# Optimization experiments

Hardware: AMD Instinct MI355X
Metric: run time of the kernel (lower is better)

The kernel has to match this reference:

```python
import jax, jax.numpy as jnp
import numpy as np

D_MODEL = 1024
NUM_HEADS = 16
HEAD_DIM = D_MODEL // NUM_HEADS
SCALE = HEAD_DIM ** -0.5
LN_EPS = 1e-5
Q_EPS = 1e-5


def bit_quant(W):
    # BitNet b1.58 ternary weight quantization with straight-through estimator.
    gamma = jnp.mean(jnp.abs(W))
    Wq = jnp.clip(jnp.round(W / (gamma + Q_EPS)), -1.0, 1.0) * gamma
    return W + jax.lax.stop_gradient(Wq - W)


def layer_norm(x, gamma, beta):
    mu = jnp.mean(x, axis=-1, keepdims=True)
    var = jnp.mean(jnp.square(x - mu), axis=-1, keepdims=True)
    return (x - mu) * jax.lax.rsqrt(var + LN_EPS) * gamma + beta


def setup_inputs() -> dict:
    key = jax.random.key(0)
    ks = jax.random.split(key, 8)
    B, T, T_ctx, C = 4, 1024, 2048, D_MODEL
    w_std = C ** -0.5
    return {
        "x": jax.random.normal(ks[0], (B, T, C), jnp.float32),
        "context": jax.random.normal(ks[1], (B, T_ctx, C), jnp.float32),
        "Wq": jax.random.normal(ks[2], (C, C), jnp.float32) * w_std,
        "bq": jnp.zeros((C,), jnp.float32),
        "Wk": jax.random.normal(ks[3], (C, C), jnp.float32) * w_std,
        "bk": jnp.zeros((C,), jnp.float32),
        "Wv": jax.random.normal(ks[4], (C, C), jnp.float32) * w_std,
        "bv": jnp.zeros((C,), jnp.float32),
        "Wo": jax.random.normal(ks[5], (C, C), jnp.float32) * w_std,
        "bo": jnp.zeros((C,), jnp.float32),
        "ln_gamma": jnp.ones((C,), jnp.float32),
        "ln_beta": jnp.zeros((C,), jnp.float32),
    }


def reference(x, context, Wq, bq, Wk, bk, Wv, bv, Wo, bo, ln_gamma, ln_beta):
    B, T, C = x.shape
    T_ctx = context.shape[1]
    residual = x
    xn = layer_norm(x, ln_gamma, ln_beta)
    # BitNet-quantized projections (torch Linear: y = x @ W.T + b)
    q = xn @ bit_quant(Wq).T + bq                      # [B,T,C]
    k = context @ bit_quant(Wk).T + bk                 # [B,T_ctx,C]
    v = context @ bit_quant(Wv).T + bv                 # [B,T_ctx,C]
    q = q.reshape(B, T, NUM_HEADS, HEAD_DIM)
    k = k.reshape(B, T_ctx, NUM_HEADS, HEAD_DIM)
    v = v.reshape(B, T_ctx, NUM_HEADS, HEAD_DIM)
    scores = jnp.einsum("bqhd,bkhd->bhqk", q, k) * SCALE   # [B,H,T,T_ctx]
    probs = jax.nn.softmax(scores, axis=-1)
    out = jnp.einsum("bhqk,bkhd->bqhd", probs, v).reshape(B, T, C)
    return residual + (out @ bit_quant(Wo).T + bo)
```

## Files before the change

kernel.cpp:

```cpp
#include <hip/hip_runtime.h>
#include <hip/hip_bf16.h>

typedef __attribute__((ext_vector_type(8))) short s8x;
typedef __attribute__((ext_vector_type(4))) float f4x;
typedef unsigned short u16;
typedef unsigned int u32;

#define T_ 1024
#define TC_ 2048
#define SCLOG2E 0.1803368801111243f

#define WAIT_VM(n) asm volatile("s_waitcnt vmcnt(" #n ")" ::: "memory")

__device__ __forceinline__ u16 f2bf(float f) {
    u32 u = __float_as_uint(f);
    return (u16)((u + 0x7fffu + ((u >> 16) & 1u)) >> 16);
}

#if defined(__has_builtin)
#if __has_builtin(__builtin_amdgcn_cvt_pk_bf16_f32)
#define HAVE_PK 1
#endif
#if __has_builtin(__builtin_amdgcn_permlane16_swap) && __has_builtin(__builtin_amdgcn_permlane32_swap)
#define HAVE_PLSWAP 1
#endif
#endif

__device__ __forceinline__ u32 pack2bf(float a, float b) {
#ifdef HAVE_PK
    typedef __attribute__((ext_vector_type(2))) __bf16 bf2t;
    bf2t r = __builtin_amdgcn_cvt_pk_bf16_f32(a, b);
    u32 u;
    __builtin_memcpy(&u, &r, 4);
    return u;
#else
    return (u32)f2bf(a) | ((u32)f2bf(b) << 16);
#endif
}

__device__ __forceinline__ void pswap32(u32& a, u32& b) {
#ifdef HAVE_PLSWAP
    typedef __attribute__((ext_vector_type(2))) unsigned int u2x;
    u2x r = __builtin_amdgcn_permlane32_swap(a, b, false, false);
    a = r.x; b = r.y;
#else
    asm("v_permlane32_swap_b32 %0, %1" : "+v"(a), "+v"(b));
#endif
}
__device__ __forceinline__ void pswap16(u32& a, u32& b) {
#ifdef HAVE_PLSWAP
    typedef __attribute__((ext_vector_type(2))) unsigned int u2x;
    u2x r = __builtin_amdgcn_permlane16_swap(a, b, false, false);
    a = r.x; b = r.y;
#else
    asm("v_permlane16_swap_b32 %0, %1" : "+v"(a), "+v"(b));
#endif
}

__device__ __forceinline__ void gload16(const void* g, void* l) {
    __builtin_amdgcn_global_load_lds((const __attribute__((address_space(1))) u32*)g,
                                     (__attribute__((address_space(3))) u32*)l, 16, 0, 0);
}

__global__ __launch_bounds__(256) void absmean_k(const float* __restrict__ W0, const float* __restrict__ W1,
                                                 const float* __restrict__ W2, const float* __restrict__ W3,
                                                 float* __restrict__ gsum) {
    int wi = blockIdx.y;
    const float* W = (wi == 0) ? W0 : (wi == 1) ? W1 : (wi == 2) ? W2 : W3;
    const int n4 = (1024 * 1024) / 4;
    float s = 0.f;
    int stride = gridDim.x * blockDim.x;
    for (int i = blockIdx.x * blockDim.x + threadIdx.x; i < n4; i += stride) {
        float4 v = ((const float4*)W)[i];
        s += fabsf(v.x) + fabsf(v.y) + fabsf(v.z) + fabsf(v.w);
    }
#pragma unroll
    for (int off = 32; off; off >>= 1) s += __shfl_down(s, off, 64);
    __shared__ float ps[4];
    if ((threadIdx.x & 63) == 0) ps[threadIdx.x >> 6] = s;
    __syncthreads();
    if (threadIdx.x == 0) atomicAdd(gsum + wi, ps[0] + ps[1] + ps[2] + ps[3]);
}

__global__ __launch_bounds__(256) void prep_k(
        const float* __restrict__ x, const float* __restrict__ lng, const float* __restrict__ lnb,
        u16* __restrict__ xn,
        const float* __restrict__ ctx, u16* __restrict__ ctxb,
        const float* __restrict__ W0, const float* __restrict__ W1,
        const float* __restrict__ W2, const float* __restrict__ W3,
        u16* __restrict__ D0, u16* __restrict__ D1, u16* __restrict__ D2, u16* __restrict__ D3,
        const float* __restrict__ gsum) {
    __shared__ float ps[8];
    int bx = blockIdx.x, t = threadIdx.x;
    if (bx < 4096) {
        int row = bx;
        float4 xv = ((const float4*)(x + (long)row * 1024))[t];
        float s = xv.x + xv.y + xv.z + xv.w;
        float s2 = xv.x * xv.x + xv.y * xv.y + xv.z * xv.z + xv.w * xv.w;
#pragma unroll
        for (int off = 32; off; off >>= 1) { s += __shfl_down(s, off, 64); s2 += __shfl_down(s2, off, 64); }
        if ((t & 63) == 0) { ps[t >> 6] = s; ps[4 + (t >> 6)] = s2; }
        __syncthreads();
        float S = ps[0] + ps[1] + ps[2] + ps[3];
        float S2 = ps[4] + ps[5] + ps[6] + ps[7];
        float mu = S * (1.f / 1024.f);
        float var = S2 * (1.f / 1024.f) - mu * mu;
        float rstd = rsqrtf(var + 1e-5f);
        float4 gv = ((const float4*)lng)[t];
        float4 bv = ((const float4*)lnb)[t];
        uint2 o;
        o.x = pack2bf((xv.x - mu) * rstd * gv.x + bv.x, (xv.y - mu) * rstd * gv.y + bv.y);
        o.y = pack2bf((xv.z - mu) * rstd * gv.z + bv.z, (xv.w - mu) * rstd * gv.w + bv.w);
        ((uint2*)(xn + (long)row * 1024))[t] = o;
    } else if (bx < 12288) {
        int i = (bx - 4096) * 256 + t;
        float4 v = ((const float4*)ctx)[i];
        uint2 o = {pack2bf(v.x, v.y), pack2bf(v.z, v.w)};
        ((uint2*)ctxb)[i] = o;
    } else {
        int wi = (bx - 12288) >> 10;
        const float* W = (wi == 0) ? W0 : (wi == 1) ? W1 : (wi == 2) ? W2 : W3;
        u16* D = (wi == 0) ? D0 : (wi == 1) ? D1 : (wi == 2) ? D2 : D3;
        float inv = 1.0f / (gsum[wi] * (1.0f / 1048576.0f) + 1e-5f);
        int i = ((bx - 12288) & 1023) * 256 + t;
        float4 wv = ((const float4*)W)[i];
        uint2 o;
        o.x = pack2bf(fminf(1.f, fmaxf(-1.f, rintf(wv.x * inv))),
                      fminf(1.f, fmaxf(-1.f, rintf(wv.y * inv))));
        o.y = pack2bf(fminf(1.f, fmaxf(-1.f, rintf(wv.z * inv))),
                      fminf(1.f, fmaxf(-1.f, rintf(wv.w * inv))));
        ((uint2*)D)[i] = o;
    }
}

__global__ __launch_bounds__(256) void gemm_fused(
        const u16* __restrict__ xn, const u16* __restrict__ ctxb,
        const u16* __restrict__ wtq, const u16* __restrict__ wtk, const u16* __restrict__ wtv,
        const float* __restrict__ bq, const float* __restrict__ bk, const float* __restrict__ bv,
        const float* __restrict__ gsum,
        u16* __restrict__ qb, u16* __restrict__ kb, u16* __restrict__ vtb) {
    __shared__ __align__(16) char smem[65536];
    int tid = threadIdx.x;
    int w = tid >> 6, l = tid & 63, lq = l & 15, lh = l >> 4;
    int wm = (w >> 1) * 64, wn = (w & 1) * 64;
    int bx = blockIdx.x;
    int xcd = bx & 7;
    int prob, m0, n0, gidx;
    const u16 *A, *Wt;
    const float* bias;
    float sc;
    if (bx < 256) {
        int local = bx >> 3;
        prob = 0; A = xn; Wt = wtq; bias = bq; sc = SCLOG2E; gidx = 0;
        m0 = (xcd * 4 + (local & 3)) * 128;
        n0 = (local >> 2) * 128;
    } else {
        int b = bx - 256;
        int local3 = b >> 3;
        int kv = local3 & 1;
        int idx = local3 >> 1;
        prob = 1 + kv; A = ctxb;
        Wt = kv ? wtv : wtk; bias = kv ? bv : bk; sc = 1.0f; gidx = 1 + kv;
        m0 = (xcd * 8 + (idx & 7)) * 128;
        n0 = (idx >> 3) * 128;
    }
    int sp = tid >> 3, ss = tid & 7;
    int st = ss ^ (sp & 7);
    int r0 = sp * 2 + (st >> 2), c0 = st & 3;
    const u16* Ag0 = A + (long)(m0 + r0) * 1024 + c0 * 8;
    const u16* Ag1 = Ag0 + 64 * 1024;
    const u16* Bg0 = Wt + (long)(n0 + r0) * 1024 + c0 * 8;
    const u16* Bg1 = Bg0 + 64 * 1024;
    int aoff[4], boff[4];
#pragma unroll
    for (int i = 0; i < 4; i++) {
        int ar = wm + i * 16 + lq, ap = ar >> 1;
        aoff[i] = ap * 128 + (((((ar & 1) << 2) | lh) ^ (ap & 7)) * 16);
        int br = wn + i * 16 + lq, bp = br >> 1;
        boff[i] = bp * 128 + (((((br & 1) << 2) | lh) ^ (bp & 7)) * 16);
    }
    f4x acc[4][4] = {};
#define STAGE_G(kt, buf)                                                   \
    {                                                                      \
        char* Ad = smem + (buf) * 32768;                                   \
        gload16(Ag0 + (kt) * 64, Ad + tid * 16);                           \
        gload16(Ag1 + (kt) * 64, Ad + 4096 + tid * 16);                    \
        gload16(Ag0 + (kt) * 64 + 32, Ad + 8192 + tid * 16);               \
        gload16(Ag1 + (kt) * 64 + 32, Ad + 12288 + tid * 16);              \
        gload16(Bg0 + (kt) * 64, Ad + 16384 + tid * 16);                   \
        gload16(Bg1 + (kt) * 64, Ad + 20480 + tid * 16);                   \
        gload16(Bg0 + (kt) * 64 + 32, Ad + 24576 + tid * 16);              \
        gload16(Bg1 + (kt) * 64 + 32, Ad + 28672 + tid * 16);              \
    }
    STAGE_G(0, 0);
    STAGE_G(1, 1);
#pragma unroll
    for (int kt = 0; kt < 16; kt++) {
        if (kt < 15) { WAIT_VM(8); } else { WAIT_VM(0); }
        __builtin_amdgcn_s_barrier();
        const char* Ac = smem + (kt & 1) * 32768;
        const char* Bc = Ac + 16384;
        s8x af[2][4], bfr[2][4];
#pragma unroll
        for (int h = 0; h < 2; h++)
#pragma unroll
            for (int i = 0; i < 4; i++) {
                af[h][i] = *(const s8x*)(Ac + h * 8192 + aoff[i]);
                bfr[h][i] = *(const s8x*)(Bc + h * 8192 + boff[i]);
            }
#pragma unroll
        for (int h = 0; h < 2; h++)
#pragma unroll
            for (int i = 0; i < 4; i++)
#pragma unroll
                for (int j = 0; j < 4; j++)
                    acc[i][j] = __builtin_amdgcn_mfma_f32_16x16x32_bf16(af[h][i], bfr[h][j], acc[i][j], 0, 0, 0);
        __builtin_amdgcn_s_barrier();
        if (kt + 2 < 16) STAGE_G(kt + 2, kt & 1);
    }
    float gamma = gsum[gidx] * (1.0f / 1048576.0f) * sc;
    if (prob < 2) {
        u16* outq = (prob == 0) ? qb : kb;
        int tshift = (prob == 0) ? 10 : 11;
        int tmask = (1 << tshift) - 1;
#pragma unroll
        for (int i = 0; i < 4; i++) {
            int gr = m0 + wm + i * 16 + lh * 4;
#pragma unroll
            for (int j = 0; j < 4; j++) {
                int gc = n0 + wn + j * 16 + lq;
                float bb = bias[gc] * sc;
                int h = gc >> 6, d = gc & 63;
#pragma unroll
                for (int r = 0; r < 4; r++) {
                    int row = gr + r;
                    int bidx = row >> tshift, tt = row & tmask;
                    outq[((((long)(bidx * 16 + h)) << tshift) + tt) * 64 + d] = f2bf(acc[i][j][r] * gamma + bb);
                }
            }
        }
    } else {
        __syncthreads();
        char* Ct = smem;
#pragma unroll
        for (int i = 0; i < 4; i++) {
            int tt = wm + i * 16 + lh * 4;
#pragma unroll
            for (int j = 0; j < 4; j++) {
                int c = wn + j * 16 + lq;
                float bb = bias[n0 + c];
                uint2 pk;
                pk.x = pack2bf(acc[i][j][0] * gamma + bb, acc[i][j][1] * gamma + bb);
                pk.y = pack2bf(acc[i][j][2] * gamma + bb, acc[i][j][3] * gamma + bb);
                int slot = (tt >> 3) ^ (c & 15);
                *(uint2*)(Ct + c * 256 + slot * 16 + (tt & 7) * 2) = pk;
            }
        }
        __syncthreads();
        int bb2 = m0 >> 11, t0 = m0 & 2047;
#pragma unroll
        for (int it = 0; it < 8; it++) {
            int e = it * 256 + tid;
            int c = e >> 4, ch = e & 15;
            int slot = ch ^ (c & 15);
            s8x v = *(const s8x*)(Ct + c * 256 + slot * 16);
            int gcg = n0 + c;
            int h = gcg >> 6, d = gcg & 63;
            *(s8x*)(vtb + ((long)((bb2 * 16 + h) * 64 + d)) * TC_ + t0 + ch * 8) = v;
        }
    }
}

__global__ __launch_bounds__(256) void gemm_o(const u16* __restrict__ A, const u16* __restrict__ Wt,
                                              const float* __restrict__ bias, const float* __restrict__ gsum,
                                              const float* __restrict__ residual, float* __restrict__ outr) {
    __shared__ __align__(16) char smem[49152];
    int tid = threadIdx.x;
    int w = tid >> 6, l = tid & 63, lq = l & 15, lh = l >> 4;
    int wm = (w >> 1) * 64, wn = (w & 1) * 32;
    int bx = blockIdx.x;
    int xcd = bx & 7, local = bx >> 3;
    int m0 = (xcd * 4 + (local & 3)) * 128;
    int n0 = (local >> 2) * 64;
    int sp = tid >> 3, ss = tid & 7;
    int st = ss ^ (sp & 7);
    int r0 = sp * 2 + (st >> 2), c0 = st & 3;
    const u16* Ag0 = A + (long)(m0 + r0) * 1024 + c0 * 8;
    const u16* Ag1 = Ag0 + 64 * 1024;
    const u16* Bg0 = Wt + (long)(n0 + r0) * 1024 + c0 * 8;
    int aoff[4], boff[2];
#pragma unroll
    for (int i = 0; i < 4; i++) {
        int ar = wm + i * 16 + lq, ap = ar >> 1;
        aoff[i] = ap * 128 + (((((ar & 1) << 2) | lh) ^ (ap & 7)) * 16);
    }
#pragma unroll
    for (int j = 0; j < 2; j++) {
        int br = wn + j * 16 + lq, bp = br >> 1;
        boff[j] = bp * 128 + (((((br & 1) << 2) | lh) ^ (bp & 7)) * 16);
    }
    f4x acc[4][2] = {};
#define STAGE_O(kt, buf)                                                   \
    {                                                                      \
        char* Ad = smem + (buf) * 24576;                                   \
        gload16(Ag0 + (kt) * 64, Ad + tid * 16);                           \
        gload16(Ag1 + (kt) * 64, Ad + 4096 + tid * 16);                    \
        gload16(Ag0 + (kt) * 64 + 32, Ad + 8192 + tid * 16);               \
        gload16(Ag1 + (kt) * 64 + 32, Ad + 12288 + tid * 16);              \
        gload16(Bg0 + (kt) * 64, Ad + 16384 + tid * 16);                   \
        gload16(Bg0 + (kt) * 64 + 32, Ad + 20480 + tid * 16);              \
    }
    STAGE_O(0, 0);
    STAGE_O(1, 1);
#pragma unroll
    for (int kt = 0; kt < 16; kt++) {
        if (kt < 15) { WAIT_VM(6); } else { WAIT_VM(0); }
        __builtin_amdgcn_s_barrier();
        const char* Ac = smem + (kt & 1) * 24576;
        const char* Bc = Ac + 16384;
        s8x af[2][4], bfr[2][2];
#pragma unroll
        for (int h = 0; h < 2; h++) {
#pragma unroll
            for (int i = 0; i < 4; i++) af[h][i] = *(const s8x*)(Ac + h * 8192 + aoff[i]);
#pragma unroll
            for (int j = 0; j < 2; j++) bfr[h][j] = *(const s8x*)(Bc + h * 4096 + boff[j]);
        }
#pragma unroll
        for (int h = 0; h < 2; h++)
#pragma unroll
            for (int i = 0; i < 4; i++)
#pragma unroll
                for (int j = 0; j < 2; j++)
                    acc[i][j] = __builtin_amdgcn_mfma_f32_16x16x32_bf16(af[h][i], bfr[h][j], acc[i][j], 0, 0, 0);
        __builtin_amdgcn_s_barrier();
        if (kt + 2 < 16) STAGE_O(kt + 2, kt & 1);
    }
    float gamma = gsum[3] * (1.0f / 1048576.0f);
#pragma unroll
    for (int i = 0; i < 4; i++) {
        int gr = m0 + wm + i * 16 + lh * 4;
#pragma unroll
        for (int j = 0; j < 2; j++) {
            int gc = n0 + wn + j * 16 + lq;
            float bb = bias[gc];
#pragma unroll
            for (int r = 0; r < 4; r++) {
                long idx = (long)(gr + r) * 1024 + gc;
                outr[idx] = residual[idx] + acc[i][j][r] * gamma + bb;
            }
        }
    }
}

__global__ __launch_bounds__(256, 2) void attn_k(const u16* __restrict__ qh, const u16* __restrict__ kh,
                                                 const u16* __restrict__ vth, u16* __restrict__ attn) {
    __shared__ __align__(16) char smem[65536];
    int tid = threadIdx.x, w = tid >> 6, l = tid & 63, lq = l & 15, lh = l >> 4;
    int bh = blockIdx.x, q0 = blockIdx.y * 128;
    const u16* qp = qh + ((long)bh * T_ + q0) * 64;
#pragma unroll
    for (int i = 0; i < 4; i++) {
        int cid = i * 256 + tid;
        int r = cid >> 3, c = (cid & 7) ^ (r & 7);
        gload16(qp + r * 64 + c * 8, smem + cid * 16);
    }
    __syncthreads();
    s8x qf[2][2];
#pragma unroll
    for (int qb = 0; qb < 2; qb++)
#pragma unroll
        for (int dh = 0; dh < 2; dh++) {
            int qrow = w * 32 + qb * 16 + lq;
            int ch = (dh * 4 + lh) ^ (qrow & 7);
            qf[qb][dh] = *(const s8x*)(smem + qrow * 128 + ch * 16);
        }
    __syncthreads();
    int sr = tid >> 3, sc = (tid & 7) ^ ((tid >> 3) & 7);
    const u16* kgA = kh + (long)bh * TC_ * 64 + sr * 64 + sc * 8;
    const u16* kgB = kgA + 2048;
    const u16* vgA = vth + (long)bh * 64 * TC_ + (long)sr * TC_ + sc * 8;
    const u16* vgB = vgA + 32 * TC_;
    const char* pA = smem + lq * 128 + ((lh ^ (lq & 7)) * 16);
    const char* pB = smem + lq * 128 + (((4 + lh) ^ (lq & 7)) * 16);
#define STAGE4(buf)                                              \
    {                                                            \
        char* Kb = smem + (buf) * 16384;                         \
        gload16(kgA, Kb + tid * 16);                             \
        gload16(kgB, Kb + 4096 + tid * 16);                      \
        gload16(vgA, Kb + 8192 + tid * 16);                      \
        gload16(vgB, Kb + 12288 + tid * 16);                     \
        kgA += 4096; kgB += 4096; vgA += 64; vgB += 64;          \
    }
#define SM1(ZA, qb, PF0, PF1)                                                                              \
    s8x PF0, PF1;                                                                                          \
    {                                                                                                      \
        u32 w00 = pack2bf(__builtin_amdgcn_exp2f(ZA[qb][0][0]), __builtin_amdgcn_exp2f(ZA[qb][0][1]));     \
        u32 w01 = pack2bf(__builtin_amdgcn_exp2f(ZA[qb][0][2]), __builtin_amdgcn_exp2f(ZA[qb][0][3]));     \
        u32 w10 = pack2bf(__builtin_amdgcn_exp2f(ZA[qb][1][0]), __builtin_amdgcn_exp2f(ZA[qb][1][1]));     \
        u32 w11 = pack2bf(__builtin_amdgcn_exp2f(ZA[qb][1][2]), __builtin_amdgcn_exp2f(ZA[qb][1][3]));     \
        u32 w20 = pack2bf(__builtin_amdgcn_exp2f(ZA[qb][2][0]), __builtin_amdgcn_exp2f(ZA[qb][2][1]));     \
        u32 w21 = pack2bf(__builtin_amdgcn_exp2f(ZA[qb][2][2]), __builtin_amdgcn_exp2f(ZA[qb][2][3]));     \
        u32 w30 = pack2bf(__builtin_amdgcn_exp2f(ZA[qb][3][0]), __builtin_amdgcn_exp2f(ZA[qb][3][1]));     \
        u32 w31 = pack2bf(__builtin_amdgcn_exp2f(ZA[qb][3][2]), __builtin_amdgcn_exp2f(ZA[qb][3][3]));     \
        u32 a0w = w00, a1w = w10; pswap32(a0w, a1w); pswap16(a0w, a1w);                                    \
        u32 b0w = w01, b1w = w11; pswap32(b0w, b1w); pswap16(b0w, b1w);                                    \
        u32 c0w = w20, c1w = w30; pswap32(c0w, c1w); pswap16(c0w, c1w);                                    \
        u32 d0w = w21, d1w = w31; pswap32(d0w, d1w); pswap16(d0w, d1w);                                    \
        u32 pw0[4] = {a0w, b0w, a1w, b1w};                                                                 \
        u32 pw1[4] = {c0w, d0w, c1w, d1w};                                                                 \
        __builtin_memcpy(&PF0, pw0, 16);                                                                   \
        __builtin_memcpy(&PF1, pw1, 16);                                                                   \
    }
#define SUBITER(JB, KB, SB, ZC, ZN, WN, DOSTAGE)                                                           \
    {                                                                                                      \
        WAIT_VM(WN);                                                                                       \
        __builtin_amdgcn_s_barrier();                                                                      \
        if (DOSTAGE) STAGE4(SB);                                                                           \
        s8x a0_[4], a1_[4], v0_[4], v1_[4];                                                                \
        _Pragma("unroll") for (int ni = 0; ni < 4; ni++) {                                                 \
            a0_[ni] = *(const s8x*)(pA + (KB) * 16384 + ni * 2048);                                        \
            a1_[ni] = *(const s8x*)(pB + (KB) * 16384 + ni * 2048);                                        \
        }                                                                                                  \
        _Pragma("unroll") for (int nd = 0; nd < 4; nd++) {                                                 \
            v0_[nd] = *(const s8x*)(pA + (JB) * 16384 + 8192 + nd * 2048);                                 \
            v1_[nd] = *(const s8x*)(pB + (JB) * 16384 + 8192 + nd * 2048);                                 \
        }                                                                                                  \
        SM1(ZC, 0, pfa0, pfa1)                                                                             \
        __builtin_amdgcn_s_setprio(1);                                                                     \
        _Pragma("unroll") for (int ni = 0; ni < 4; ni++) {                                                 \
            _Pragma("unroll") for (int qb = 0; qb < 2; qb++) {                                             \
                f4x zz = {0.f, 0.f, 0.f, 0.f};                                                             \
                zz = __builtin_amdgcn_mfma_f32_16x16x32_bf16(a0_[ni], qf[qb][0], zz, 0, 0, 0);             \
                zz = __builtin_amdgcn_mfma_f32_16x16x32_bf16(a1_[ni], qf[qb][1], zz, 0, 0, 0);             \
                ZN[qb][ni] = zz;                                                                           \
            }                                                                                              \
        }                                                                                                  \
        __builtin_amdgcn_s_setprio(0);                                                                     \
        SM1(ZC, 1, pfb0, pfb1)                                                                             \
        __builtin_amdgcn_s_setprio(1);                                                                     \
        lrun[0] = __builtin_amdgcn_mfma_f32_16x16x32_bf16(pfa0, ones, lrun[0], 0, 0, 0);                   \
        lrun[0] = __builtin_amdgcn_mfma_f32_16x16x32_bf16(pfa1, ones, lrun[0], 0, 0, 0);                   \
        lrun[1] = __builtin_amdgcn_mfma_f32_16x16x32_bf16(pfb0, ones, lrun[1], 0, 0, 0);                   \
        lrun[1] = __builtin_amdgcn_mfma_f32_16x16x32_bf16(pfb1, ones, lrun[1], 0, 0, 0);                   \
        _Pragma("unroll") for (int nd = 0; nd < 4; nd++) {                                                 \
            oacc[0][nd] = __builtin_amdgcn_mfma_f32_16x16x32_bf16(pfa0, v0_[nd], oacc[0][nd], 0, 0, 0);    \
            oacc[0][nd] = __builtin_amdgcn_mfma_f32_16x16x32_bf16(pfa1, v1_[nd], oacc[0][nd], 0, 0, 0);    \
            oacc[1][nd] = __builtin_amdgcn_mfma_f32_16x16x32_bf16(pfb0, v0_[nd], oacc[1][nd], 0, 0, 0);    \
            oacc[1][nd] = __builtin_amdgcn_mfma_f32_16x16x32_bf16(pfb1, v1_[nd], oacc[1][nd], 0, 0, 0);    \
        }                                                                                                  \
        __builtin_amdgcn_s_setprio(0);                                                                     \
    }
    const s8x ones = {16256, 16256, 16256, 16256, 16256, 16256, 16256, 16256};
    f4x z0[2][4], z1[2][4];
    f4x oacc[2][4] = {};
    f4x lrun[2] = {};
    STAGE4(0); STAGE4(1); STAGE4(2);
    WAIT_VM(8);
    __builtin_amdgcn_s_barrier();
    {
        s8x a0_[4], a1_[4];
#pragma unroll
        for (int ni = 0; ni < 4; ni++) {
            a0_[ni] = *(const s8x*)(pA + ni * 2048);
            a1_[ni] = *(const s8x*)(pB + ni * 2048);
        }
#pragma unroll
        for (int ni = 0; ni < 4; ni++)
#pragma unroll
            for (int qb = 0; qb < 2; qb++) {
                f4x zz = {0.f, 0.f, 0.f, 0.f};
                zz = __builtin_amdgcn_mfma_f32_16x16x32_bf16(a0_[ni], qf[qb][0], zz, 0, 0, 0);
                zz = __builtin_amdgcn_mfma_f32_16x16x32_bf16(a1_[ni], qf[qb][1], zz, 0, 0, 0);
                z0[qb][ni] = zz;
            }
    }
    for (int t = 0; t < 7; t++) {
        SUBITER(0, 1, 3, z0, z1, 4, true)
        SUBITER(1, 2, 0, z1, z0, 4, true)
        SUBITER(2, 3, 1, z0, z1, 4, true)
        SUBITER(3, 0, 2, z1, z0, 4, true)
    }
    SUBITER(0, 1, 3, z0, z1, 4, true)
    SUBITER(1, 2, 0, z1, z0, 4, false)
    SUBITER(2, 3, 1, z0, z1, 0, false)
    {
        s8x v0_[4], v1_[4];
#pragma unroll
        for (int nd = 0; nd < 4; nd++) {
            v0_[nd] = *(const s8x*)(pA + 3 * 16384 + 8192 + nd * 2048);
            v1_[nd] = *(const s8x*)(pB + 3 * 16384 + 8192 + nd * 2048);
        }
        SM1(z1, 0, pfa0, pfa1)
        SM1(z1, 1, pfb0, pfb1)
        __builtin_amdgcn_s_setprio(1);
        lrun[0] = __builtin_amdgcn_mfma_f32_16x16x32_bf16(pfa0, ones, lrun[0], 0, 0, 0);
        lrun[0] = __builtin_amdgcn_mfma_f32_16x16x32_bf16(pfa1, ones, lrun[0], 0, 0, 0);
        lrun[1] = __builtin_amdgcn_mfma_f32_16x16x32_bf16(pfb0, ones, lrun[1], 0, 0, 0);
        lrun[1] = __builtin_amdgcn_mfma_f32_16x16x32_bf16(pfb1, ones, lrun[1], 0, 0, 0);
#pragma unroll
        for (int nd = 0; nd < 4; nd++) {
            oacc[0][nd] = __builtin_amdgcn_mfma_f32_16x16x32_bf16(pfa0, v0_[nd], oacc[0][nd], 0, 0, 0);
            oacc[0][nd] = __builtin_amdgcn_mfma_f32_16x16x32_bf16(pfa1, v1_[nd], oacc[0][nd], 0, 0, 0);
            oacc[1][nd] = __builtin_amdgcn_mfma_f32_16x16x32_bf16(pfb0, v0_[nd], oacc[1][nd], 0, 0, 0);
            oacc[1][nd] = __builtin_amdgcn_mfma_f32_16x16x32_bf16(pfb1, v1_[nd], oacc[1][nd], 0, 0, 0);
        }
        __builtin_amdgcn_s_setprio(0);
    }
    int b = bh >> 4, h = bh & 15;
#pragma unroll
    for (int qb = 0; qb < 2; qb++)
#pragma unroll
        for (int r = 0; r < 4; r++) {
            int q = q0 + w * 32 + qb * 16 + lh * 4 + r;
            float rcp = 1.f / lrun[qb][r];
#pragma unroll
            for (int nd = 0; nd < 4; nd++)
                attn[((long)(b * T_ + q)) * 1024 + h * 64 + nd * 16 + lq] = f2bf(oacc[qb][nd][r] * rcp);
        }
}

extern "C" void kernel_launch(void* const* d_in, const int* in_sizes, int n_in,
                              void* d_out, int out_size, void* d_ws, size_t ws_size,
                              hipStream_t stream) {
    const float* x   = (const float*)d_in[0];
    const float* ctx = (const float*)d_in[1];
    const float* Wq  = (const float*)d_in[2];
    const float* bq  = (const float*)d_in[3];
    const float* Wk  = (const float*)d_in[4];
    const float* bk  = (const float*)d_in[5];
    const float* Wv  = (const float*)d_in[6];
    const float* bv  = (const float*)d_in[7];
    const float* Wo  = (const float*)d_in[8];
    const float* bo  = (const float*)d_in[9];
    const float* lng = (const float*)d_in[10];
    const float* lnb = (const float*)d_in[11];
    float* out = (float*)d_out;

    char* ws = (char*)d_ws;
    float* gsum = (float*)ws;
    size_t off = 256;
    u16* wtq  = (u16*)(ws + off); off += (size_t)1024 * 1024 * 2;
    u16* wtk  = (u16*)(ws + off); off += (size_t)1024 * 1024 * 2;
    u16* wtv  = (u16*)(ws + off); off += (size_t)1024 * 1024 * 2;
    u16* wto  = (u16*)(ws + off); off += (size_t)1024 * 1024 * 2;
    u16* ctxb = (u16*)(ws + off); off += (size_t)8192 * 1024 * 2;
    u16* xn   = (u16*)(ws + off); off += (size_t)4096 * 1024 * 2;
    u16* qb_  = (u16*)(ws + off); off += (size_t)4096 * 1024 * 2;
    u16* kb   = (u16*)(ws + off); off += (size_t)8192 * 1024 * 2;
    u16* vtb  = (u16*)(ws + off); off += (size_t)8192 * 1024 * 2;
    u16* attnb = xn;

    hipMemsetAsync(gsum, 0, 16, stream);
    absmean_k<<<dim3(128, 4), 256, 0, stream>>>(Wq, Wk, Wv, Wo, gsum);
    prep_k<<<16384, 256, 0, stream>>>(x, lng, lnb, xn, ctx, ctxb,
                                      Wq, Wk, Wv, Wo, wtq, wtk, wtv, wto, gsum);
    gemm_fused<<<1280, 256, 0, stream>>>(xn, ctxb, wtq, wtk, wtv, bq, bk, bv, gsum, qb_, kb, vtb);
    attn_k<<<dim3(64, 8), 256, 0, stream>>>(qb_, kb, vtb, attnb);
    gemm_o<<<512, 256, 0, stream>>>(attnb, wto, bo, gsum, x, out);
}
```

Before: 233.1 us.

## Load K fragments directly from global into registers, staging only V in LDS

```diff
diff --git a/kernel.cpp b/kernel.cpp
--- a/kernel.cpp
+++ b/kernel.cpp
@@ -355,7 +355,7 @@
 
 __global__ __launch_bounds__(256, 2) void attn_k(const u16* __restrict__ qh, const u16* __restrict__ kh,
                                                  const u16* __restrict__ vth, u16* __restrict__ attn) {
-    __shared__ __align__(16) char smem[65536];
+    __shared__ __align__(16) char smem[24576];
     int tid = threadIdx.x, w = tid >> 6, l = tid & 63, lq = l & 15, lh = l >> 4;
     int bh = blockIdx.x, q0 = blockIdx.y * 128;
     const u16* qp = qh + ((long)bh * T_ + q0) * 64;
@@ -377,20 +377,30 @@
         }
     __syncthreads();
     int sr = tid >> 3, sc = (tid & 7) ^ ((tid >> 3) & 7);
-    const u16* kgA = kh + (long)bh * TC_ * 64 + sr * 64 + sc * 8;
-    const u16* kgB = kgA + 2048;
     const u16* vgA = vth + (long)bh * 64 * TC_ + (long)sr * TC_ + sc * 8;
     const u16* vgB = vgA + 32 * TC_;
+    const u16* kfA = kh + (long)bh * TC_ * 64 + lq * 64 + lh * 8;
+    const u16* kf2 = kfA + 2048;
     const char* pA = smem + lq * 128 + ((lh ^ (lq & 7)) * 16);
     const char* pB = smem + lq * 128 + (((4 + lh) ^ (lq & 7)) * 16);
-#define STAGE4(buf)                                              \
+#define STAGE_V(buf)                                             \
     {                                                            \
-        char* Kb = smem + (buf) * 16384;                         \
-        gload16(kgA, Kb + tid * 16);                             \
-        gload16(kgB, Kb + 4096 + tid * 16);                      \
-        gload16(vgA, Kb + 8192 + tid * 16);                      \
-        gload16(vgB, Kb + 12288 + tid * 16);                     \
-        kgA += 4096; kgB += 4096; vgA += 64; vgB += 64;          \
+        char* Vb = smem + (buf) * 8192;                          \
+        gload16(vgA, Vb + tid * 16);                             \
+        gload16(vgB, Vb + 4096 + tid * 16);                      \
+        vgA += 64; vgB += 64;                                    \
+    }
+#define KLOAD(KA, KB_)                                           \
+    {                                                            \
+        KA[0]  = *(const s8x*)(kfA);                             \
+        KA[1]  = *(const s8x*)(kfA + 1024);                      \
+        KA[2]  = *(const s8x*)(kf2);                             \
+        KA[3]  = *(const s8x*)(kf2 + 1024);                      \
+        KB_[0] = *(const s8x*)(kfA + 32);                        \
+        KB_[1] = *(const s8x*)(kfA + 1056);                      \
+        KB_[2] = *(const s8x*)(kf2 + 32);                        \
+        KB_[3] = *(const s8x*)(kf2 + 1056);                      \
+        kfA += 4096; kf2 += 4096;                                \
     }
 #define SM1(ZA, qb, PF0, PF1)                                                                              \
     s8x PF0, PF1;                                                                                          \
@@ -412,27 +422,23 @@
         __builtin_memcpy(&PF0, pw0, 16);                                                                   \
         __builtin_memcpy(&PF1, pw1, 16);                                                                   \
     }
-#define SUBITER(JB, KB, SB, ZC, ZN, WN, DOSTAGE)                                                           \
+#define SUBITER(JB, SB, ZC, ZN, KCa, KCb, KNa, KNb, WN, DOSK)                                              \
     {                                                                                                      \
         WAIT_VM(WN);                                                                                       \
         __builtin_amdgcn_s_barrier();                                                                      \
-        if (DOSTAGE) STAGE4(SB);                                                                           \
-        s8x a0_[4], a1_[4], v0_[4], v1_[4];                                                                \
-        _Pragma("unroll") for (int ni = 0; ni < 4; ni++) {                                                 \
-            a0_[ni] = *(const s8x*)(pA + (KB) * 16384 + ni * 2048);                                        \
-            a1_[ni] = *(const s8x*)(pB + (KB) * 16384 + ni * 2048);                                        \
-        }                                                                                                  \
+        if (DOSK) { STAGE_V(SB); KLOAD(KNa, KNb); }                                                        \
+        s8x v0_[4], v1_[4];                                                                                \
         _Pragma("unroll") for (int nd = 0; nd < 4; nd++) {                                                 \
-            v0_[nd] = *(const s8x*)(pA + (JB) * 16384 + 8192 + nd * 2048);                                 \
-            v1_[nd] = *(const s8x*)(pB + (JB) * 16384 + 8192 + nd * 2048);                                 \
+            v0_[nd] = *(const s8x*)(pA + (JB) * 8192 + nd * 2048);                                         \
+            v1_[nd] = *(const s8x*)(pB + (JB) * 8192 + nd * 2048);                                         \
         }                                                                                                  \
         SM1(ZC, 0, pfa0, pfa1)                                                                             \
         __builtin_amdgcn_s_setprio(1);                                                                     \
         _Pragma("unroll") for (int ni = 0; ni < 4; ni++) {                                                 \
             _Pragma("unroll") for (int qb = 0; qb < 2; qb++) {                                             \
                 f4x zz = {0.f, 0.f, 0.f, 0.f};                                                             \
-                zz = __builtin_amdgcn_mfma_f32_16x16x32_bf16(a0_[ni], qf[qb][0], zz, 0, 0, 0);             \
-                zz = __builtin_amdgcn_mfma_f32_16x16x32_bf16(a1_[ni], qf[qb][1], zz, 0, 0, 0);             \
+                zz = __builtin_amdgcn_mfma_f32_16x16x32_bf16(KCa[ni], qf[qb][0], zz, 0, 0, 0);             \
+                zz = __builtin_amdgcn_mfma_f32_16x16x32_bf16(KCb[ni], qf[qb][1], zz, 0, 0, 0);             \
                 ZN[qb][ni] = zz;                                                                           \
             }                                                                                              \
         }                                                                                                  \
@@ -452,44 +458,41 @@
         __builtin_amdgcn_s_setprio(0);                                                                     \
     }
     const s8x ones = {16256, 16256, 16256, 16256, 16256, 16256, 16256, 16256};
+    s8x kXa[4], kXb[4], kYa[4], kYb[4];
     f4x z0[2][4], z1[2][4];
     f4x oacc[2][4] = {};
     f4x lrun[2] = {};
-    STAGE4(0); STAGE4(1); STAGE4(2);
-    WAIT_VM(8);
-    __builtin_amdgcn_s_barrier();
+    STAGE_V(0); STAGE_V(1);
+    KLOAD(kXa, kXb);
+    KLOAD(kYa, kYb);
     {
-        s8x a0_[4], a1_[4];
-#pragma unroll
-        for (int ni = 0; ni < 4; ni++) {
-            a0_[ni] = *(const s8x*)(pA + ni * 2048);
-            a1_[ni] = *(const s8x*)(pB + ni * 2048);
-        }
 #pragma unroll
         for (int ni = 0; ni < 4; ni++)
 #pragma unroll
             for (int qb = 0; qb < 2; qb++) {
                 f4x zz = {0.f, 0.f, 0.f, 0.f};
-                zz = __builtin_amdgcn_mfma_f32_16x16x32_bf16(a0_[ni], qf[qb][0], zz, 0, 0, 0);
-                zz = __builtin_amdgcn_mfma_f32_16x16x32_bf16(a1_[ni], qf[qb][1], zz, 0, 0, 0);
+                zz = __builtin_amdgcn_mfma_f32_16x16x32_bf16(kXa[ni], qf[qb][0], zz, 0, 0, 0);
+                zz = __builtin_amdgcn_mfma_f32_16x16x32_bf16(kXb[ni], qf[qb][1], zz, 0, 0, 0);
                 z0[qb][ni] = zz;
             }
     }
-    for (int t = 0; t < 7; t++) {
-        SUBITER(0, 1, 3, z0, z1, 4, true)
-        SUBITER(1, 2, 0, z1, z0, 4, true)
-        SUBITER(2, 3, 1, z0, z1, 4, true)
-        SUBITER(3, 0, 2, z1, z0, 4, true)
-    }
-    SUBITER(0, 1, 3, z0, z1, 4, true)
-    SUBITER(1, 2, 0, z1, z0, 4, false)
-    SUBITER(2, 3, 1, z0, z1, 0, false)
+    for (int t = 0; t < 5; t++) {
+        SUBITER(0, 2, z0, z1, kYa, kYb, kXa, kXb, 10, true)
+        SUBITER(1, 0, z1, z0, kXa, kXb, kYa, kYb, 10, true)
+        SUBITER(2, 1, z0, z1, kYa, kYb, kXa, kXb, 10, true)
+        SUBITER(0, 2, z1, z0, kXa, kXb, kYa, kYb, 10, true)
+        SUBITER(1, 0, z0, z1, kYa, kYb, kXa, kXb, 10, true)
+        SUBITER(2, 1, z1, z0, kXa, kXb, kYa, kYb, 10, true)
+    }
+    SUBITER(0, 2, z0, z1, kYa, kYb, kXa, kXb, 10, false)
     {
+        WAIT_VM(8);
+        __builtin_amdgcn_s_barrier();
         s8x v0_[4], v1_[4];
 #pragma unroll
         for (int nd = 0; nd < 4; nd++) {
-            v0_[nd] = *(const s8x*)(pA + 3 * 16384 + 8192 + nd * 2048);
-            v1_[nd] = *(const s8x*)(pB + 3 * 16384 + 8192 + nd * 2048);
+            v0_[nd] = *(const s8x*)(pA + 1 * 8192 + nd * 2048);
+            v1_[nd] = *(const s8x*)(pB + 1 * 8192 + nd * 2048);
         }
         SM1(z1, 0, pfa0, pfa1)
         SM1(z1, 1, pfb0, pfb1)
```

After: 261.1 us. +12.1%, slower.
